# Optimization experiments

Hardware: AMD Instinct MI355X
Metric: run time of the kernel (lower is better)

The kernel has to match this reference:

```python
import jax, jax.numpy as jnp
import numpy as np
import math

B, D, K = 256, 128, 4096
OUTPUT_SIZE = 1281167
T = 0.07


def setup_inputs() -> dict:
    key = jax.random.key(0)
    k1, k2, k3, k4 = jax.random.split(key, 4)
    x = jax.random.normal(k1, (B, D), dtype=jnp.float32)
    y = jax.random.randint(k2, (B,), 0, OUTPUT_SIZE, dtype=jnp.int64)
    idx = jax.random.randint(k3, (B, K + 1), 0, OUTPUT_SIZE, dtype=jnp.int64)
    stdv = 1.0 / math.sqrt(D / 3.0)
    memory = jax.random.uniform(k4, (OUTPUT_SIZE, D), dtype=jnp.float32,
                                minval=-stdv, maxval=stdv)
    return {"x": x, "y": y, "idx": idx, "memory": memory}


def reference(x, y, idx, memory):
    outputSize = memory.shape[0]
    # first column of idx is overwritten with the positive index y
    idx = idx.at[:, 0].set(y)
    # gather K+1 rows per sample from the memory bank: (B, K+1, D)
    weight = memory[idx]
    # batched dot product: (B, K+1)
    logits = jnp.einsum('bkd,bd->bk', weight, x) / T
    e = jnp.exp(logits)
    # Z is set on first call from the batch statistics (params[2] == -1 path)
    Z = e.mean() * outputSize
    out = e / Z
    return out
```

## Files before the change

kernel.cpp:

```cpp
#include <hip/hip_runtime.h>


constexpr int   kB        = 256;
constexpr int   kKp1      = 4097;
constexpr long long kOutRows = 1281167LL;
constexpr int   kSplits   = 8;
constexpr int   kMainBlocks = kB * kSplits;
constexpr int   kThreads  = 256;
constexpr float kInvT     = 1.0f / 0.07f;

__global__ __launch_bounds__(kThreads) void nce_main(
    const float* __restrict__ x, const int* __restrict__ y,
    const int* __restrict__ idx, const float* __restrict__ memory,
    float* __restrict__ out, float* __restrict__ blksum)
{
    const int b     = blockIdx.x / kSplits;
    const int chunk = blockIdx.x % kSplits;
    const int tid   = threadIdx.x;
    const int wave  = tid >> 6;
    const int lane  = tid & 63;
    const int half  = lane >> 5;
    const int dlane = lane & 31;
    const int slot  = wave * 2 + half;

    const float4* x4 = reinterpret_cast<const float4*>(x) + (size_t)b * 32;
    const float4  xv = x4[dlane];

    const float4* m4   = reinterpret_cast<const float4*>(memory);
    const int*    idxb = idx + (size_t)b * kKp1;
    float*        outb = out + (size_t)b * kKp1;

    const int per = (kKp1 + kSplits - 1) / kSplits;
    const int k0  = chunk * per;
    const int k1  = (k0 + per < kKp1) ? (k0 + per) : kKp1;

    float acc = 0.0f;
    for (int k = k0 + slot; k < k1; k += 8) {
        const int row = (k == 0) ? y[b] : idxb[k];
        const float4 mv = m4[(size_t)row * 32 + dlane];
        float dot = mv.x * xv.x + mv.y * xv.y + mv.z * xv.z + mv.w * xv.w;
        #pragma unroll
        for (int m = 16; m >= 1; m >>= 1)
            dot += __shfl_xor(dot, m, 64);
        const float e = __expf(dot * kInvT);
        if (dlane == 0) {
            outb[k] = e;
            acc += e;
        }
    }

    #pragma unroll
    for (int m = 32; m >= 1; m >>= 1)
        acc += __shfl_xor(acc, m, 64);
    __shared__ float red[kThreads / 64];
    if (lane == 0) red[wave] = acc;
    __syncthreads();
    if (tid == 0)
        blksum[blockIdx.x] = red[0] + red[1] + red[2] + red[3];
}

__global__ __launch_bounds__(256) void nce_scale(float* __restrict__ blksum)
{
    float s = 0.0f;
    for (int i = threadIdx.x; i < kMainBlocks; i += 256) s += blksum[i];
    #pragma unroll
    for (int m = 32; m >= 1; m >>= 1)
        s += __shfl_xor(s, m, 64);
    __shared__ float red[4];
    const int wave = threadIdx.x >> 6;
    if ((threadIdx.x & 63) == 0) red[wave] = s;
    __syncthreads();
    if (threadIdx.x == 0) {
        const float tot = red[0] + red[1] + red[2] + red[3];
        const float scale = ((float)(kB * kKp1) / (float)kOutRows) / tot;
        blksum[kMainBlocks] = scale;
    }
}

__global__ __launch_bounds__(256) void nce_norm(
    float4* __restrict__ out4, const float* __restrict__ scalep, int n4)
{
    const float sc = scalep[0];
    int i = blockIdx.x * blockDim.x + threadIdx.x;
    const int stride = gridDim.x * blockDim.x;
    for (; i < n4; i += stride) {
        float4 v = out4[i];
        v.x *= sc; v.y *= sc; v.z *= sc; v.w *= sc;
        out4[i] = v;
    }
}

extern "C" void kernel_launch(void* const* d_in, const int* in_sizes, int n_in,
                              void* d_out, int out_size, void* d_ws, size_t ws_size,
                              hipStream_t stream) {
    const float* x      = (const float*)d_in[0];
    const int*   y      = (const int*)d_in[1];
    const int*   idx    = (const int*)d_in[2];
    const float* memory = (const float*)d_in[3];
    float*       out    = (float*)d_out;
    float*       blksum = (float*)d_ws;

    hipLaunchKernelGGL(nce_main, dim3(kMainBlocks), dim3(kThreads), 0, stream,
                       x, y, idx, memory, out, blksum);
    hipLaunchKernelGGL(nce_scale, dim3(1), dim3(256), 0, stream, blksum);
    hipLaunchKernelGGL(nce_norm, dim3(1024), dim3(256), 0, stream,
                       (float4*)d_out, blksum + kMainBlocks, out_size / 4);
}
```

Baseline: 105.2 us.

## Batch four gathered rows per half-wave and fold scale reduction into normalize kernel

Each half-wave now loads four index values and four memory rows before reducing, so more independent gathers are in flight per thread and the latency-bound random row fetches can overlap. The shuffle reductions for the four dots are interleaved. The separate single-block scale kernel is removed. Every block of the normalize kernel now redundantly reduces the 2048 block sums itself, which saves one launch but adds repeated small reads.

```diff
diff --git a/kernel.cpp b/kernel.cpp
--- a/kernel.cpp
+++ b/kernel.cpp
@@ -1,51 +1,71 @@
 #include <hip/hip_runtime.h>
 
 
-constexpr int   kB        = 256;
-constexpr int   kKp1      = 4097;
+constexpr int   kB          = 256;
+constexpr int   kKp1        = 4097;
 constexpr long long kOutRows = 1281167LL;
-constexpr int   kSplits   = 8;
+constexpr int   kSplits     = 8;
 constexpr int   kMainBlocks = kB * kSplits;
-constexpr int   kThreads  = 256;
-constexpr float kInvT     = 1.0f / 0.07f;
+constexpr int   kThreads    = 256;
+constexpr float kInvT       = 1.0f / 0.07f;
+
+__device__ __forceinline__ float dot4(float4 a, float4 b) {
+    return a.x * b.x + a.y * b.y + a.z * b.z + a.w * b.w;
+}
 
 __global__ __launch_bounds__(kThreads) void nce_main(
     const float* __restrict__ x, const int* __restrict__ y,
     const int* __restrict__ idx, const float* __restrict__ memory,
     float* __restrict__ out, float* __restrict__ blksum)
 {
-    const int b     = blockIdx.x / kSplits;
-    const int chunk = blockIdx.x % kSplits;
+    const int b     = blockIdx.x >> 3;
+    const int chunk = blockIdx.x & 7;
     const int tid   = threadIdx.x;
     const int wave  = tid >> 6;
     const int lane  = tid & 63;
     const int half  = lane >> 5;
     const int dlane = lane & 31;
-    const int slot  = wave * 2 + half;
+    const int g     = wave * 2 + half;
 
-    const float4* x4 = reinterpret_cast<const float4*>(x) + (size_t)b * 32;
-    const float4  xv = x4[dlane];
-
+    const float4 xv = reinterpret_cast<const float4*>(x)[b * 32 + dlane];
     const float4* m4   = reinterpret_cast<const float4*>(memory);
     const int*    idxb = idx + (size_t)b * kKp1;
     float*        outb = out + (size_t)b * kKp1;
+    const int     ypos = y[b];
 
     const int per = (kKp1 + kSplits - 1) / kSplits;
     const int k0  = chunk * per;
     const int k1  = (k0 + per < kKp1) ? (k0 + per) : kKp1;
 
     float acc = 0.0f;
-    for (int k = k0 + slot; k < k1; k += 8) {
-        const int row = (k == 0) ? y[b] : idxb[k];
-        const float4 mv = m4[(size_t)row * 32 + dlane];
-        float dot = mv.x * xv.x + mv.y * xv.y + mv.z * xv.z + mv.w * xv.w;
+    for (int kb = k0 + g * 4; kb < k1; kb += 32) {
+        const int krem = k1 - kb;
+        const int r0 = (kb == 0) ? ypos : idxb[kb];
+        const int r1 = (krem > 1) ? idxb[kb + 1] : 0;
+        const int r2 = (krem > 2) ? idxb[kb + 2] : 0;
+        const int r3 = (krem > 3) ? idxb[kb + 3] : 0;
+        const float4 a0 = m4[(size_t)r0 * 32 + dlane];
+        const float4 a1 = m4[(size_t)r1 * 32 + dlane];
+        const float4 a2 = m4[(size_t)r2 * 32 + dlane];
+        const float4 a3 = m4[(size_t)r3 * 32 + dlane];
+        float d0 = dot4(a0, xv), d1 = dot4(a1, xv);
+        float d2 = dot4(a2, xv), d3 = dot4(a3, xv);
         #pragma unroll
-        for (int m = 16; m >= 1; m >>= 1)
-            dot += __shfl_xor(dot, m, 64);
-        const float e = __expf(dot * kInvT);
+        for (int m = 16; m >= 1; m >>= 1) {
+            d0 += __shfl_xor(d0, m, 64);
+            d1 += __shfl_xor(d1, m, 64);
+            d2 += __shfl_xor(d2, m, 64);
+            d3 += __shfl_xor(d3, m, 64);
+        }
         if (dlane == 0) {
-            outb[k] = e;
-            acc += e;
+            const float e0 = __expf(d0 * kInvT);
+            const float e1 = __expf(d1 * kInvT);
+            const float e2 = __expf(d2 * kInvT);
+            const float e3 = __expf(d3 * kInvT);
+            outb[kb] = e0;  acc += e0;
+            if (krem > 1) { outb[kb + 1] = e1; acc += e1; }
+            if (krem > 2) { outb[kb + 2] = e2; acc += e2; }
+            if (krem > 3) { outb[kb + 3] = e3; acc += e3; }
         }
     }
 
@@ -59,7 +79,8 @@
         blksum[blockIdx.x] = red[0] + red[1] + red[2] + red[3];
 }
 
-__global__ __launch_bounds__(256) void nce_scale(float* __restrict__ blksum)
+__global__ __launch_bounds__(256) void nce_norm(
+    float4* __restrict__ out4, const float* __restrict__ blksum, int n4)
 {
     float s = 0.0f;
     for (int i = threadIdx.x; i < kMainBlocks; i += 256) s += blksum[i];
@@ -67,20 +88,11 @@
     for (int m = 32; m >= 1; m >>= 1)
         s += __shfl_xor(s, m, 64);
     __shared__ float red[4];
-    const int wave = threadIdx.x >> 6;
-    if ((threadIdx.x & 63) == 0) red[wave] = s;
+    if ((threadIdx.x & 63) == 0) red[threadIdx.x >> 6] = s;
     __syncthreads();
-    if (threadIdx.x == 0) {
-        const float tot = red[0] + red[1] + red[2] + red[3];
-        const float scale = ((float)(kB * kKp1) / (float)kOutRows) / tot;
-        blksum[kMainBlocks] = scale;
-    }
-}
+    const float tot = red[0] + red[1] + red[2] + red[3];
+    const float sc = ((float)(kB * kKp1) / (float)kOutRows) / tot;
 
-__global__ __launch_bounds__(256) void nce_norm(
-    float4* __restrict__ out4, const float* __restrict__ scalep, int n4)
-{
-    const float sc = scalep[0];
     int i = blockIdx.x * blockDim.x + threadIdx.x;
     const int stride = gridDim.x * blockDim.x;
     for (; i < n4; i += stride) {
@@ -102,7 +114,6 @@
 
     hipLaunchKernelGGL(nce_main, dim3(kMainBlocks), dim3(kThreads), 0, stream,
                        x, y, idx, memory, out, blksum);
-    hipLaunchKernelGGL(nce_scale, dim3(1), dim3(256), 0, stream, blksum);
     hipLaunchKernelGGL(nce_norm, dim3(1024), dim3(256), 0, stream,
-                       (float4*)d_out, blksum + kMainBlocks, out_size / 4);
+                       (float4*)d_out, blksum, out_size / 4);
 }
```

Measured after the change: 91.21 us. -13.3%, faster.
